# Kernel optimization log

Measured on AMD Instinct MI355X. Metric: run time of the kernel, lower is better.

The kernel has to match this reference:

```python
import jax, jax.numpy as jnp
import numpy as np

N = 100000   # nodes
E = 1600000  # edges (before self loops)
D = 128      # input_dim
H1 = 128     # hidden_dim_1
H2 = 128     # hidden_dim_2
OUT = 1      # output_dim
G = 64       # number of graphs in the batch


def setup_inputs() -> dict:
    key = jax.random.key(0)
    ks = jax.random.split(key, 11)
    x = jax.random.normal(ks[0], (N, D), dtype=jnp.float32)
    edge_index = jax.random.randint(ks[1], (2, E), 0, N, dtype=jnp.int64)
    batch = jnp.sort(jax.random.randint(ks[2], (N,), 0, G, dtype=jnp.int64))
    s = 0.05
    W1 = jax.random.normal(ks[3], (D, H1), dtype=jnp.float32) * s
    b1 = jnp.zeros((H1,), dtype=jnp.float32)
    W2 = jax.random.normal(ks[4], (H1, H2), dtype=jnp.float32) * s
    b2 = jnp.zeros((H2,), dtype=jnp.float32)
    W_iou = jax.random.normal(ks[5], (H2, OUT), dtype=jnp.float32) * s
    b_iou = jnp.zeros((OUT,), dtype=jnp.float32)
    W_iop = jax.random.normal(ks[6], (H2, OUT), dtype=jnp.float32) * s
    b_iop = jnp.zeros((OUT,), dtype=jnp.float32)
    return dict(x=x, edge_index=edge_index, batch=batch,
                W1=W1, b1=b1, W2=W2, b2=b2,
                W_iou=W_iou, b_iou=b_iou, W_iop=W_iop, b_iop=b_iop)


def reference(x, edge_index, batch, W1, b1, W2, b2, W_iou, b_iou, W_iop, b_iop):
    n = x.shape[0]
    # add_self_loops
    loops = jnp.arange(n, dtype=edge_index.dtype)
    src = jnp.concatenate([edge_index[0], loops])
    dst = jnp.concatenate([edge_index[1], loops])
    # symmetric GCN normalization: deg over target nodes
    deg = jax.ops.segment_sum(jnp.ones_like(dst, dtype=x.dtype), dst, num_segments=n)
    dinv = jnp.where(deg > 0, jax.lax.rsqrt(deg), 0.0)
    norm = dinv[src] * dinv[dst]  # [E+N]

    def gcn_conv(h, W, b):
        hw = h @ W                                  # [N, H]
        m = hw[src] * norm[:, None]                 # gather + normalize [E+N, H]
        return jax.ops.segment_sum(m, dst, num_segments=n) + b  # scatter-add

    h = jax.nn.relu(gcn_conv(x, W1, b1))
    h = jax.nn.relu(gcn_conv(h, W2, b2))
    # global_max_pool over graph ids
    pooled = jax.ops.segment_max(h, batch, num_segments=G)
    pooled = jnp.where(jnp.isfinite(pooled), pooled, 0.0)  # guard empty graphs
    iou = pooled @ W_iou + b_iou
    iop = pooled @ W_iop + b_iop
    return jnp.concatenate([iou, iop], axis=1)  # [G, 2*OUT]
```

## Files before the change

### kernel.cpp

```cpp
#include <hip/hip_runtime.h>
#include <math.h>

typedef unsigned int u32;
typedef __attribute__((ext_vector_type(8))) short short8v;
typedef __attribute__((ext_vector_type(4))) float floatx4;

__device__ inline int rfl(int v) { return __builtin_amdgcn_readfirstlane(v); }

__device__ inline float blo(u32 u) { return __uint_as_float(u << 16); }
__device__ inline float bhi(u32 u) { return __uint_as_float(u & 0xffff0000u); }
__device__ inline u32 f2b(float f) {
    u32 u = __float_as_uint(f);
    return (u + 0x7fffu + ((u >> 16) & 1u)) >> 16;
}
__device__ inline u32 pack2(float a, float b) { return f2b(a) | (f2b(b) << 16); }

__global__ void init_k(u32* gcursor, int B, int CAP, u32* pooled, int np) {
    int i = blockIdx.x * blockDim.x + threadIdx.x;
    if (i < np) pooled[i] = 0u;
    if (i < B) gcursor[i] = (u32)i * (u32)CAP;
}

__global__ __launch_bounds__(256) void wprep_k(const float* __restrict__ W1, const float* __restrict__ W2,
                                               ushort* __restrict__ W1t, ushort* __restrict__ W2t) {
    int idx = blockIdx.x * 256 + threadIdx.x;
    int k = idx >> 7, j = idx & 127;
    W1t[j * 128 + k] = (ushort)f2b(W1[idx]);
    W2t[j * 128 + k] = (ushort)f2b(W2[idx]);
}

#define FILL_EPT 16
__global__ __launch_bounds__(256) void bfill_k(const int* __restrict__ src, const int* __restrict__ dst,
                                               u32* __restrict__ gcursor, u32* __restrict__ pairs,
                                               int E, int B, int CAP) {
    __shared__ u32 lcnt[256];
    __shared__ u32 lbase[256];
    const int t = threadIdx.x;
    lcnt[t] = 0;
    __syncthreads();

    const int base_e = blockIdx.x * (256 * FILL_EPT);
    u32 pk[FILL_EPT];
    u32 bk[FILL_EPT];
    u32 rk[FILL_EPT];
#pragma unroll
    for (int j = 0; j < FILL_EPT; ++j) {
        int e = base_e + t + j * 256;
        pk[j] = 0xFFFFFFFFu;
        if (e < E) {
            int d = dst[e];
            int s = src[e];
            u32 b = (u32)d >> 9;
            pk[j] = (u32)s | (((u32)d & 511u) << 17);
            bk[j] = b;
            rk[j] = atomicAdd(&lcnt[b], 1u);
        }
    }
    __syncthreads();
    if (t < B) {
        u32 v = lcnt[t];
        lbase[t] = v ? atomicAdd(&gcursor[t], v) : 0u;
    }
    __syncthreads();
#pragma unroll
    for (int j = 0; j < FILL_EPT; ++j) {
        if (pk[j] != 0xFFFFFFFFu) {
            u32 b = bk[j];
            u32 pos = lbase[b] + rk[j];
            if (pos < (b + 1u) * (u32)CAP) pairs[pos] = pk[j];
        }
    }
}

__global__ __launch_bounds__(256) void csort_k(const u32* __restrict__ pairs, const u32* __restrict__ gcursor,
                                               u32* __restrict__ csr, uint2* __restrict__ rowinfo,
                                               float* __restrict__ dinv, int N, int CAP) {
    __shared__ u32 hist[512];
    __shared__ u32 excl[512];
    __shared__ u32 pscan[256];
    const int b = blockIdx.x, t = threadIdx.x;
    const u32 base = (u32)b * (u32)CAP;
    u32 cnt = gcursor[b] - base;
    if (cnt > (u32)CAP) cnt = (u32)CAP;

    hist[t] = 0u; hist[t + 256] = 0u;
    __syncthreads();
    for (u32 j = t; j < cnt; j += 256) {
        u32 p = pairs[base + j];
        atomicAdd(&hist[p >> 17], 1u);
    }
    __syncthreads();
    u32 a = hist[2 * t], c = hist[2 * t + 1];
    u32 s = a + c;
    pscan[t] = s;
    __syncthreads();
    for (int off = 1; off < 256; off <<= 1) {
        u32 v = (t >= off) ? pscan[t - off] : 0u;
        __syncthreads();
        pscan[t] += v;
        __syncthreads();
    }
    u32 e0 = pscan[t] - s;
    excl[2 * t] = e0;
    excl[2 * t + 1] = e0 + a;
    __syncthreads();
    const int node0 = b << 9;
#pragma unroll
    for (int q = 0; q < 2; ++q) {
        int loc = t + q * 256;
        int i = node0 + loc;
        if (i < N) {
            u32 dg = hist[loc];
            rowinfo[i] = make_uint2(base + excl[loc], dg);
            dinv[i] = rsqrtf((float)(dg + 1u));
        }
    }
    __syncthreads();
    for (u32 j = t; j < cnt; j += 256) {
        u32 p = pairs[base + j];
        u32 loc = p >> 17;
        u32 pos = atomicAdd(&excl[loc], 1u);
        csr[base + pos] = p & 0x1FFFFu;
    }
}

__device__ inline int swz(int row, int kbyte) { return row * 256 + (kbyte ^ ((row & 7) << 4)); }

template <bool BF16IN>
__global__ __launch_bounds__(256) void gemm_mfma_k(const void* __restrict__ inp, const ushort* __restrict__ Wt,
                                                   const float* __restrict__ dinv,
                                                   ushort* __restrict__ outp, int N) {
    __shared__ char Wl[128 * 256];
    const int t = threadIdx.x;
    const int brow = blockIdx.x * 128;

    {
        const uint4* g = (const uint4*)Wt;
#pragma unroll
        for (int i = 0; i < 8; ++i) {
            int f = t + i * 256;
            int r = f >> 4, kb = (f & 15) << 4;
            *(uint4*)(Wl + swz(r, kb)) = g[f];
        }
    }

    const int lane = t & 63;
    const int wave = t >> 6;
    const int l15 = lane & 15;
    const int g4 = lane >> 4;

    short8v a[2][4];
#pragma unroll
    for (int mt = 0; mt < 2; ++mt) {
        int row = brow + wave * 32 + mt * 16 + l15;
        bool ok = row < N;
        int rowc = ok ? row : 0;
#pragma unroll
        for (int ks = 0; ks < 4; ++ks) {
            uint4 v = make_uint4(0u, 0u, 0u, 0u);
            if (BF16IN) {
                if (ok) v = *(const uint4*)((const char*)inp + (size_t)rowc * 256 + (ks * 64 + g4 * 16));
            } else {
                if (ok) {
                    const float4* p = (const float4*)((const char*)inp + (size_t)rowc * 512 + (ks * 128 + g4 * 32));
                    float4 x0 = p[0], x1 = p[1];
                    v = make_uint4(pack2(x0.x, x0.y), pack2(x0.z, x0.w), pack2(x1.x, x1.y), pack2(x1.z, x1.w));
                }
            }
            a[mt][ks] = *(short8v*)&v;
        }
    }
    __syncthreads();

    floatx4 acc[2][8];
#pragma unroll
    for (int mt = 0; mt < 2; ++mt)
#pragma unroll
        for (int nt = 0; nt < 8; ++nt) acc[mt][nt] = (floatx4){0.f, 0.f, 0.f, 0.f};

#pragma unroll
    for (int ks = 0; ks < 4; ++ks) {
        int kb = ks * 64 + g4 * 16;
        short8v b[8];
#pragma unroll
        for (int nt = 0; nt < 8; ++nt)
            b[nt] = *(const short8v*)(Wl + swz(nt * 16 + l15, kb));
#pragma unroll
        for (int mt = 0; mt < 2; ++mt)
#pragma unroll
            for (int nt = 0; nt < 8; ++nt)
                acc[mt][nt] = __builtin_amdgcn_mfma_f32_16x16x32_bf16(a[mt][ks], b[nt], acc[mt][nt], 0, 0, 0);
    }

    const int r0w = g4 * 4;
#pragma unroll
    for (int mt = 0; mt < 2; ++mt) {
#pragma unroll
        for (int reg = 0; reg < 4; ++reg) {
            int grow = brow + wave * 32 + mt * 16 + r0w + reg;
            if (grow < N) {
                float sc = dinv[grow];
#pragma unroll
                for (int nt = 0; nt < 8; ++nt)
                    outp[grow * 128 + nt * 16 + l15] = (ushort)f2b(acc[mt][nt][reg] * sc);
            }
        }
    }
}

__global__ __launch_bounds__(256) void edge_accum_k(const u32* __restrict__ hw, const uint2* __restrict__ rowinfo,
                                                    const u32* __restrict__ csr, const float* __restrict__ dinv,
                                                    const float* __restrict__ bias, u32* __restrict__ hout, int N) {
    const int lane = threadIdx.x & 63;
    const int wid = (blockIdx.x * blockDim.x + threadIdx.x) >> 6;
    const int nw = (gridDim.x * blockDim.x) >> 6;
    const float2 bb = ((const float2*)bias)[lane];

    for (int i = wid; i < N; i += nw) {
        uint2 ri = rowinfo[i];
        const int r0 = rfl((int)ri.x);
        const int deg = rfl((int)ri.y);
        float di = dinv[i];
        u32 us = hw[(size_t)i * 64 + lane];
        float a0 = blo(us), a1 = bhi(us);

        int j = 0;
        for (; j + 8 <= deg; j += 8) {
            int s0 = rfl((int)csr[r0 + j + 0]);
            int s1 = rfl((int)csr[r0 + j + 1]);
            int s2 = rfl((int)csr[r0 + j + 2]);
            int s3 = rfl((int)csr[r0 + j + 3]);
            int s4 = rfl((int)csr[r0 + j + 4]);
            int s5 = rfl((int)csr[r0 + j + 5]);
            int s6 = rfl((int)csr[r0 + j + 6]);
            int s7 = rfl((int)csr[r0 + j + 7]);
            u32 u0 = hw[(size_t)s0 * 64 + lane];
            u32 u1 = hw[(size_t)s1 * 64 + lane];
            u32 u2 = hw[(size_t)s2 * 64 + lane];
            u32 u3 = hw[(size_t)s3 * 64 + lane];
            u32 u4 = hw[(size_t)s4 * 64 + lane];
            u32 u5 = hw[(size_t)s5 * 64 + lane];
            u32 u6 = hw[(size_t)s6 * 64 + lane];
            u32 u7 = hw[(size_t)s7 * 64 + lane];
            a0 += blo(u0); a1 += bhi(u0);
            a0 += blo(u1); a1 += bhi(u1);
            a0 += blo(u2); a1 += bhi(u2);
            a0 += blo(u3); a1 += bhi(u3);
            a0 += blo(u4); a1 += bhi(u4);
            a0 += blo(u5); a1 += bhi(u5);
            a0 += blo(u6); a1 += bhi(u6);
            a0 += blo(u7); a1 += bhi(u7);
        }
        if (j < deg) {
            const int rem = deg - j;
#pragma unroll
            for (int k = 0; k < 8; ++k) {
                int off = (k < rem) ? k : (rem - 1);
                int s = rfl((int)csr[r0 + j + off]);
                u32 u = hw[(size_t)s * 64 + lane];
                float v0 = (k < rem) ? blo(u) : 0.f;
                float v1 = (k < rem) ? bhi(u) : 0.f;
                a0 += v0; a1 += v1;
            }
        }

        a0 = fmaxf(fmaf(a0, di, bb.x), 0.f);
        a1 = fmaxf(fmaf(a1, di, bb.y), 0.f);
        hout[(size_t)i * 64 + lane] = pack2(a0, a1);
    }
}

__global__ __launch_bounds__(64) void pool_k(const u32* __restrict__ h2, const int* __restrict__ batch,
                                             u32* __restrict__ pooled, int N) {
    int lane = threadIdx.x;
    int start = blockIdx.x * 64;
    int end = min(start + 64, N);
    if (start >= N) return;
    int gcur = batch[start];
    float m0 = 0.f, m1 = 0.f;
    for (int n = start; n < end; ++n) {
        int g = batch[n];
        if (g != gcur) {
            atomicMax(pooled + gcur * 128 + lane * 2, __float_as_uint(m0));
            atomicMax(pooled + gcur * 128 + lane * 2 + 1, __float_as_uint(m1));
            gcur = g;
            m0 = m1 = 0.f;
        }
        u32 u = h2[n * 64 + lane];
        m0 = fmaxf(m0, blo(u));
        m1 = fmaxf(m1, bhi(u));
    }
    atomicMax(pooled + gcur * 128 + lane * 2, __float_as_uint(m0));
    atomicMax(pooled + gcur * 128 + lane * 2 + 1, __float_as_uint(m1));
}

__global__ void final_k(const float* __restrict__ pooled, const float* __restrict__ Wu, const float* __restrict__ bu,
                        const float* __restrict__ Wp, const float* __restrict__ bp, float* __restrict__ out) {
    int t = threadIdx.x;
    int g = t >> 1, c = t & 1;
    const float* w = c ? Wp : Wu;
    const float* pr = pooled + g * 128;
    float s = 0.f;
    for (int k = 0; k < 128; k += 4)
        s += pr[k] * w[k] + pr[k + 1] * w[k + 1] + pr[k + 2] * w[k + 2] + pr[k + 3] * w[k + 3];
    out[g * 2 + c] = s + (c ? bp[0] : bu[0]);
}

extern "C" void kernel_launch(void* const* d_in, const int* in_sizes, int n_in,
                              void* d_out, int out_size, void* d_ws, size_t ws_size,
                              hipStream_t stream) {
    const float* x     = (const float*)d_in[0];
    const int*   ei    = (const int*)d_in[1];
    const int*   batch = (const int*)d_in[2];
    const float* W1    = (const float*)d_in[3];
    const float* b1    = (const float*)d_in[4];
    const float* W2    = (const float*)d_in[5];
    const float* b2    = (const float*)d_in[6];
    const float* Wu    = (const float*)d_in[7];
    const float* bu    = (const float*)d_in[8];
    const float* Wp    = (const float*)d_in[9];
    const float* bp    = (const float*)d_in[10];
    float* out = (float*)d_out;

    const int N = in_sizes[2];
    const int E = in_sizes[1] / 2;
    const int* src = ei;
    const int* dst = ei + E;

    const int B = (N + 511) >> 9;
    int avg = E / B;
    int CAP = avg + 6 * (int)sqrt((double)avg) + 64;
    CAP = (CAP + 63) & ~63;

    char* ws = (char*)d_ws;
    size_t o = 0;
    auto alloc = [&](size_t bytes) { size_t r = o; o += (bytes + 255) & ~(size_t)255; return r; };
    u32*   gcursor = (u32*)(ws + alloc(1024));
    float* dinv    = (float*)(ws + alloc((size_t)N * 4));
    uint2* rowinfo = (uint2*)(ws + alloc((size_t)N * 8));
    u32*   csr     = (u32*)(ws + alloc((size_t)B * CAP * 4));
    ushort* hwA    = (ushort*)(ws + alloc((size_t)N * 128 * 2));
    ushort* hwB    = (ushort*)(ws + alloc((size_t)N * 128 * 2));
    u32*   pooled  = (u32*)(ws + alloc(64 * 128 * 4));
    ushort* W1t    = (ushort*)(ws + alloc(128 * 128 * 2));
    ushort* W2t    = (ushort*)(ws + alloc(128 * 128 * 2));
    u32*   pairs   = (u32*)hwA;
    (void)ws_size; (void)n_in;

    const int gFill = (E + 256 * FILL_EPT - 1) / (256 * FILL_EPT);
    const int gGemm = (N + 127) / 128;
    const int gPool = (N + 63) / 64;

    init_k<<<32, 256, 0, stream>>>(gcursor, B, CAP, pooled, 64 * 128);
    wprep_k<<<64, 256, 0, stream>>>(W1, W2, W1t, W2t);
    bfill_k<<<gFill, 256, 0, stream>>>(src, dst, gcursor, pairs, E, B, CAP);
    csort_k<<<B, 256, 0, stream>>>(pairs, gcursor, csr, rowinfo, dinv, N, CAP);

    gemm_mfma_k<false><<<gGemm, 256, 0, stream>>>((const void*)x, W1t, dinv, hwA, N);
    edge_accum_k<<<2048, 256, 0, stream>>>((const u32*)hwA, rowinfo, csr, dinv, b1, (u32*)hwB, N);
    gemm_mfma_k<true><<<gGemm, 256, 0, stream>>>((const void*)hwB, W2t, dinv, hwA, N);
    edge_accum_k<<<2048, 256, 0, stream>>>((const u32*)hwA, rowinfo, csr, dinv, b2, (u32*)hwB, N);

    pool_k<<<gPool, 64, 0, stream>>>((const u32*)hwB, batch, pooled, N);
    final_k<<<1, 128, 0, stream>>>((const float*)pooled, Wu, bu, Wp, bp, out);
}
```

Baseline: 238.0 us.

## Fuse second aggregation with max-pool, merge init kernels, vectorize bucket fill

The second GCN aggregation now feeds a running per-graph max directly instead of writing h2 and launching a separate pool kernel, so the N×128 bf16 round trip and one launch go away. The init and weight-prep kernels are merged into one launch. Bucket fill reads src/dst as int4. The counting sort now runs 512 threads, one per node slot, with a single scan. Waves that span several graphs issue extra atomics, and a wave whose range lies within one graph still emits one atomicMax per lane at the end.

```diff
diff --git a/kernel.cpp b/kernel.cpp
--- a/kernel.cpp
+++ b/kernel.cpp
@@ -15,18 +15,15 @@
 }
 __device__ inline u32 pack2(float a, float b) { return f2b(a) | (f2b(b) << 16); }
 
-__global__ void init_k(u32* gcursor, int B, int CAP, u32* pooled, int np) {
-    int i = blockIdx.x * blockDim.x + threadIdx.x;
-    if (i < np) pooled[i] = 0u;
-    if (i < B) gcursor[i] = (u32)i * (u32)CAP;
-}
-
-__global__ __launch_bounds__(256) void wprep_k(const float* __restrict__ W1, const float* __restrict__ W2,
-                                               ushort* __restrict__ W1t, ushort* __restrict__ W2t) {
+__global__ __launch_bounds__(256) void prep_k(const float* __restrict__ W1, const float* __restrict__ W2,
+                                              ushort* __restrict__ W1t, ushort* __restrict__ W2t,
+                                              u32* __restrict__ gcursor, int B, int CAP, u32* __restrict__ pooled) {
     int idx = blockIdx.x * 256 + threadIdx.x;
     int k = idx >> 7, j = idx & 127;
     W1t[j * 128 + k] = (ushort)f2b(W1[idx]);
     W2t[j * 128 + k] = (ushort)f2b(W2[idx]);
+    if (idx < 64 * 128) pooled[idx] = 0u;
+    if (idx < B) gcursor[idx] = (u32)idx * (u32)CAP;
 }
 
 #define FILL_EPT 16
@@ -44,16 +41,35 @@
     u32 bk[FILL_EPT];
     u32 rk[FILL_EPT];
 #pragma unroll
-    for (int j = 0; j < FILL_EPT; ++j) {
-        int e = base_e + t + j * 256;
-        pk[j] = 0xFFFFFFFFu;
-        if (e < E) {
-            int d = dst[e];
-            int s = src[e];
-            u32 b = (u32)d >> 9;
-            pk[j] = (u32)s | (((u32)d & 511u) << 17);
-            bk[j] = b;
-            rk[j] = atomicAdd(&lcnt[b], 1u);
+    for (int q = 0; q < FILL_EPT / 4; ++q) {
+        int e0 = base_e + (q * 256 + t) * 4;
+        if (e0 + 3 < E) {
+            int4 s4 = *(const int4*)(src + e0);
+            int4 d4 = *(const int4*)(dst + e0);
+            int ss[4] = {s4.x, s4.y, s4.z, s4.w};
+            int dd[4] = {d4.x, d4.y, d4.z, d4.w};
+#pragma unroll
+            for (int r = 0; r < 4; ++r) {
+                int j = q * 4 + r;
+                u32 b = (u32)dd[r] >> 9;
+                pk[j] = (u32)ss[r] | (((u32)dd[r] & 511u) << 17);
+                bk[j] = b;
+                rk[j] = atomicAdd(&lcnt[b], 1u);
+            }
+        } else {
+#pragma unroll
+            for (int r = 0; r < 4; ++r) {
+                int j = q * 4 + r;
+                int e = e0 + r;
+                pk[j] = 0xFFFFFFFFu;
+                if (e < E) {
+                    int d = dst[e];
+                    u32 b = (u32)d >> 9;
+                    pk[j] = (u32)src[e] | (((u32)d & 511u) << 17);
+                    bk[j] = b;
+                    rk[j] = atomicAdd(&lcnt[b], 1u);
+                }
+            }
         }
     }
     __syncthreads();
@@ -72,54 +88,46 @@
     }
 }
 
-__global__ __launch_bounds__(256) void csort_k(const u32* __restrict__ pairs, const u32* __restrict__ gcursor,
+__global__ __launch_bounds__(512) void csort_k(const u32* __restrict__ pairs, const u32* __restrict__ gcursor,
                                                u32* __restrict__ csr, uint2* __restrict__ rowinfo,
                                                float* __restrict__ dinv, int N, int CAP) {
     __shared__ u32 hist[512];
-    __shared__ u32 excl[512];
-    __shared__ u32 pscan[256];
+    __shared__ u32 scanb[512];
     const int b = blockIdx.x, t = threadIdx.x;
     const u32 base = (u32)b * (u32)CAP;
     u32 cnt = gcursor[b] - base;
     if (cnt > (u32)CAP) cnt = (u32)CAP;
 
-    hist[t] = 0u; hist[t + 256] = 0u;
-    __syncthreads();
-    for (u32 j = t; j < cnt; j += 256) {
+    hist[t] = 0u;
+    __syncthreads();
+    for (u32 j = t; j < cnt; j += 512) {
         u32 p = pairs[base + j];
         atomicAdd(&hist[p >> 17], 1u);
     }
     __syncthreads();
-    u32 a = hist[2 * t], c = hist[2 * t + 1];
-    u32 s = a + c;
-    pscan[t] = s;
-    __syncthreads();
-    for (int off = 1; off < 256; off <<= 1) {
-        u32 v = (t >= off) ? pscan[t - off] : 0u;
+    u32 v = hist[t];
+    scanb[t] = v;
+    __syncthreads();
+    for (int off = 1; off < 512; off <<= 1) {
+        u32 x = (t >= off) ? scanb[t - off] : 0u;
         __syncthreads();
-        pscan[t] += v;
+        scanb[t] += x;
         __syncthreads();
     }
-    u32 e0 = pscan[t] - s;
-    excl[2 * t] = e0;
-    excl[2 * t + 1] = e0 + a;
-    __syncthreads();
-    const int node0 = b << 9;
-#pragma unroll
-    for (int q = 0; q < 2; ++q) {
-        int loc = t + q * 256;
-        int i = node0 + loc;
-        if (i < N) {
-            u32 dg = hist[loc];
-            rowinfo[i] = make_uint2(base + excl[loc], dg);
-            dinv[i] = rsqrtf((float)(dg + 1u));
-        }
-    }
-    __syncthreads();
-    for (u32 j = t; j < cnt; j += 256) {
+    u32 excl_t = scanb[t] - v;
+
+    int i = (b << 9) + t;
+    if (i < N) {
+        rowinfo[i] = make_uint2(base + excl_t, v);
+        dinv[i] = rsqrtf((float)(v + 1u));
+    }
+    __syncthreads();
+    hist[t] = excl_t;
+    __syncthreads();
+    for (u32 j = t; j < cnt; j += 512) {
         u32 p = pairs[base + j];
         u32 loc = p >> 17;
-        u32 pos = atomicAdd(&excl[loc], 1u);
+        u32 pos = atomicAdd(&hist[loc], 1u);
         csr[base + pos] = p & 0x1FFFFu;
     }
 }
@@ -270,28 +278,84 @@
     }
 }
 
-__global__ __launch_bounds__(64) void pool_k(const u32* __restrict__ h2, const int* __restrict__ batch,
-                                             u32* __restrict__ pooled, int N) {
-    int lane = threadIdx.x;
-    int start = blockIdx.x * 64;
-    int end = min(start + 64, N);
-    if (start >= N) return;
-    int gcur = batch[start];
+__global__ __launch_bounds__(256) void edge_pool_k(const u32* __restrict__ hw, const uint2* __restrict__ rowinfo,
+                                                   const u32* __restrict__ csr, const float* __restrict__ dinv,
+                                                   const float* __restrict__ bias, const int* __restrict__ batch,
+                                                   u32* __restrict__ pooled, int N, int chunk) {
+    const int lane = threadIdx.x & 63;
+    const int gwid = (blockIdx.x * blockDim.x + threadIdx.x) >> 6;
+    const float2 bb = ((const float2*)bias)[lane];
+
+    int i0 = gwid * chunk, i1 = min(N, i0 + chunk);
     float m0 = 0.f, m1 = 0.f;
-    for (int n = start; n < end; ++n) {
-        int g = batch[n];
+    int gcur = -1;
+    for (int i = i0; i < i1; ++i) {
+        uint2 ri = rowinfo[i];
+        const int r0 = rfl((int)ri.x);
+        const int deg = rfl((int)ri.y);
+        float di = dinv[i];
+        u32 us = hw[(size_t)i * 64 + lane];
+        float a0 = blo(us), a1 = bhi(us);
+
+        int j = 0;
+        for (; j + 8 <= deg; j += 8) {
+            int s0 = rfl((int)csr[r0 + j + 0]);
+            int s1 = rfl((int)csr[r0 + j + 1]);
+            int s2 = rfl((int)csr[r0 + j + 2]);
+            int s3 = rfl((int)csr[r0 + j + 3]);
+            int s4 = rfl((int)csr[r0 + j + 4]);
+            int s5 = rfl((int)csr[r0 + j + 5]);
+            int s6 = rfl((int)csr[r0 + j + 6]);
+            int s7 = rfl((int)csr[r0 + j + 7]);
+            u32 u0 = hw[(size_t)s0 * 64 + lane];
+            u32 u1 = hw[(size_t)s1 * 64 + lane];
+            u32 u2 = hw[(size_t)s2 * 64 + lane];
+            u32 u3 = hw[(size_t)s3 * 64 + lane];
+            u32 u4 = hw[(size_t)s4 * 64 + lane];
+            u32 u5 = hw[(size_t)s5 * 64 + lane];
+            u32 u6 = hw[(size_t)s6 * 64 + lane];
+            u32 u7 = hw[(size_t)s7 * 64 + lane];
+            a0 += blo(u0); a1 += bhi(u0);
+            a0 += blo(u1); a1 += bhi(u1);
+            a0 += blo(u2); a1 += bhi(u2);
+            a0 += blo(u3); a1 += bhi(u3);
+            a0 += blo(u4); a1 += bhi(u4);
+            a0 += blo(u5); a1 += bhi(u5);
+            a0 += blo(u6); a1 += bhi(u6);
+            a0 += blo(u7); a1 += bhi(u7);
+        }
+        if (j < deg) {
+            const int rem = deg - j;
+#pragma unroll
+            for (int k = 0; k < 8; ++k) {
+                int off = (k < rem) ? k : (rem - 1);
+                int s = rfl((int)csr[r0 + j + off]);
+                u32 u = hw[(size_t)s * 64 + lane];
+                float v0 = (k < rem) ? blo(u) : 0.f;
+                float v1 = (k < rem) ? bhi(u) : 0.f;
+                a0 += v0; a1 += v1;
+            }
+        }
+
+        a0 = fmaxf(fmaf(a0, di, bb.x), 0.f);
+        a1 = fmaxf(fmaf(a1, di, bb.y), 0.f);
+
+        int g = batch[i];
         if (g != gcur) {
-            atomicMax(pooled + gcur * 128 + lane * 2, __float_as_uint(m0));
-            atomicMax(pooled + gcur * 128 + lane * 2 + 1, __float_as_uint(m1));
+            if (gcur >= 0) {
+                atomicMax(pooled + gcur * 128 + lane * 2,     __float_as_uint(m0));
+                atomicMax(pooled + gcur * 128 + lane * 2 + 1, __float_as_uint(m1));
+            }
             gcur = g;
             m0 = m1 = 0.f;
         }
-        u32 u = h2[n * 64 + lane];
-        m0 = fmaxf(m0, blo(u));
-        m1 = fmaxf(m1, bhi(u));
-    }
-    atomicMax(pooled + gcur * 128 + lane * 2, __float_as_uint(m0));
-    atomicMax(pooled + gcur * 128 + lane * 2 + 1, __float_as_uint(m1));
+        m0 = fmaxf(m0, a0);
+        m1 = fmaxf(m1, a1);
+    }
+    if (gcur >= 0) {
+        atomicMax(pooled + gcur * 128 + lane * 2,     __float_as_uint(m0));
+        atomicMax(pooled + gcur * 128 + lane * 2 + 1, __float_as_uint(m1));
+    }
 }
 
 __global__ void final_k(const float* __restrict__ pooled, const float* __restrict__ Wu, const float* __restrict__ bu,
@@ -349,18 +413,17 @@
 
     const int gFill = (E + 256 * FILL_EPT - 1) / (256 * FILL_EPT);
     const int gGemm = (N + 127) / 128;
-    const int gPool = (N + 63) / 64;
-
-    init_k<<<32, 256, 0, stream>>>(gcursor, B, CAP, pooled, 64 * 128);
-    wprep_k<<<64, 256, 0, stream>>>(W1, W2, W1t, W2t);
+    const int nWaves = 2048 * 4;
+    const int chunk = (N + nWaves - 1) / nWaves;
+
+    prep_k<<<64, 256, 0, stream>>>(W1, W2, W1t, W2t, gcursor, B, CAP, pooled);
     bfill_k<<<gFill, 256, 0, stream>>>(src, dst, gcursor, pairs, E, B, CAP);
-    csort_k<<<B, 256, 0, stream>>>(pairs, gcursor, csr, rowinfo, dinv, N, CAP);
+    csort_k<<<B, 512, 0, stream>>>(pairs, gcursor, csr, rowinfo, dinv, N, CAP);
 
     gemm_mfma_k<false><<<gGemm, 256, 0, stream>>>((const void*)x, W1t, dinv, hwA, N);
     edge_accum_k<<<2048, 256, 0, stream>>>((const u32*)hwA, rowinfo, csr, dinv, b1, (u32*)hwB, N);
     gemm_mfma_k<true><<<gGemm, 256, 0, stream>>>((const void*)hwB, W2t, dinv, hwA, N);
-    edge_accum_k<<<2048, 256, 0, stream>>>((const u32*)hwA, rowinfo, csr, dinv, b2, (u32*)hwB, N);
-
-    pool_k<<<gPool, 64, 0, stream>>>((const u32*)hwB, batch, pooled, N);
+    edge_pool_k<<<2048, 256, 0, stream>>>((const u32*)hwA, rowinfo, csr, dinv, b2, batch, pooled, N, chunk);
+
     final_k<<<1, 128, 0, stream>>>((const float*)pooled, Wu, bu, Wp, bp, out);
 }
```

Result: faster. 206.5 us (-13.3%).
